# Kernel tuning notes

Hardware: AMD Instinct MI355X
Metric: run time of the kernel (lower is better)

The kernel has to match this reference:

```python
import jax, jax.numpy as jnp
import numpy as np

N = 100000
IN_F, C1, C2, C3, OUT_F = 64, 64, 64, 64, 8


def setup_inputs() -> dict:
    key = jax.random.key(0)
    ks = jax.random.split(key, 12)
    x = jax.random.normal(ks[0], (N, IN_F), dtype=jnp.float32)
    edge_index = jax.random.randint(ks[1], (2, 1600000), 0, N, dtype=jnp.int64)

    def lin(kw, kb, fi, fo):
        s = 1.0 / np.sqrt(fi)
        W = jax.random.uniform(kw, (fi, fo), jnp.float32, -s, s)
        b = jax.random.uniform(kb, (fo,), jnp.float32, -s, s)
        return W, b

    W1, b1 = lin(ks[2], ks[3], IN_F, C1)
    W2, b2 = lin(ks[4], ks[5], C1, C2)
    W3, b3 = lin(ks[6], ks[7], C2, C3)
    Wl, bl = lin(ks[8], ks[9], C3, OUT_F)
    return {"x": x, "edge_index": edge_index, "W1": W1, "b1": b1,
            "W2": W2, "b2": b2, "W3": W3, "b3": b3, "Wl": Wl, "bl": bl}


def _gcn_norm(edge_index, n):
    # add self loops, compute symmetric normalization D^-1/2 A D^-1/2
    loops = jnp.arange(n, dtype=edge_index.dtype)
    src = jnp.concatenate([edge_index[0], loops])
    dst = jnp.concatenate([edge_index[1], loops])
    deg = jax.ops.segment_sum(jnp.ones_like(dst, dtype=jnp.float32), dst, num_segments=n)
    dis = jnp.where(deg > 0, jax.lax.rsqrt(deg), 0.0)
    norm = dis[src] * dis[dst]  # [E+N]
    return src, dst, norm


def _gcn_layer(h, W, b, src, dst, norm, n):
    h = h @ W                                   # [N, Fout] small GEMM
    msg = h[src] * norm[:, None]                # gather + scale, [E+N, Fout]
    agg = jax.ops.segment_sum(msg, dst, num_segments=n)  # scatter-add
    return agg + b


def reference(x, edge_index, W1, b1, W2, b2, W3, b3, Wl, bl):
    n = x.shape[0]
    src, dst, norm = _gcn_norm(edge_index, n)
    h = jax.nn.relu(_gcn_layer(x, W1, b1, src, dst, norm, n))
    h = jax.nn.relu(_gcn_layer(h, W2, b2, src, dst, norm, n))
    h = jax.nn.relu(_gcn_layer(h, W3, b3, src, dst, norm, n))
    return h @ Wl + bl
```

## Files before the change

kernel.cpp:

```cpp
#include <hip/hip_runtime.h>
#include <hip/hip_fp16.h>

#define F 64
#define CHUNK 2048
#define BN 512
#define BSHIFT 9
#define CAP 20480

typedef int v4i __attribute__((ext_vector_type(4)));
typedef float fx4 __attribute__((ext_vector_type(4)));
typedef float v2f __attribute__((ext_vector_type(2)));
typedef _Float16 h8f __attribute__((ext_vector_type(8)));

union FB8 { uint4 u; h8f h; };
union FX4P { fx4 v; v2f p[2]; };

__global__ __launch_bounds__(256) void k_blkcnt(const int* __restrict__ dst,
                                                int* __restrict__ blkcnt,
                                                int E, int NB, int NBKT) {
    __shared__ int lcnt[256];
    int b = blockIdx.x, t = threadIdx.x;
    lcnt[t] = 0;
    __syncthreads();
    const v4i* d4 = (const v4i*)dst;
    int g0 = (b * CHUNK) >> 2;
    int E4 = E >> 2;
#pragma unroll
    for (int k = 0; k < 2; ++k) {
        int gi = g0 + k * 256 + t;
        if (gi < E4) {
            v4i q = __builtin_nontemporal_load(d4 + gi);
            atomicAdd(&lcnt[q.x >> BSHIFT], 1);
            atomicAdd(&lcnt[q.y >> BSHIFT], 1);
            atomicAdd(&lcnt[q.z >> BSHIFT], 1);
            atomicAdd(&lcnt[q.w >> BSHIFT], 1);
        }
    }
    __syncthreads();
    if (t < NBKT) blkcnt[t * NB + b] = lcnt[t];
}

__global__ __launch_bounds__(256) void k_bktscan(const int* __restrict__ blkcnt,
                                                 int* __restrict__ blkoff,
                                                 int* __restrict__ bkttot, int NB) {
    __shared__ int s[256];
    __shared__ int running;
    int seg = blockIdx.x;
    int t = threadIdx.x;
    if (t == 0) running = 0;
    __syncthreads();
    for (int base = 0; base < NB; base += 256) {
        int i = base + t;
        int v = (i < NB) ? blkcnt[seg * NB + i] : 0;
        s[t] = v;
        __syncthreads();
        for (int off = 1; off < 256; off <<= 1) {
            int x = (t >= off) ? s[t - off] : 0;
            __syncthreads();
            s[t] += x;
            __syncthreads();
        }
        int rbase = running;
        if (i < NB) blkoff[seg * NB + i] = rbase + s[t] - v;
        int ctot = s[255];
        __syncthreads();
        if (t == 0) running = rbase + ctot;
        __syncthreads();
    }
    if (t == 0) bkttot[seg] = running;
}

__global__ void k_sb(const int* __restrict__ bkttot, int* __restrict__ sb, int NBKT) {
    __shared__ int s[256];
    int t = threadIdx.x;
    int v = (t < NBKT) ? bkttot[t] : 0;
    s[t] = v;
    __syncthreads();
    for (int off = 1; off < 256; off <<= 1) {
        int x = (t >= off) ? s[t - off] : 0;
        __syncthreads();
        s[t] += x;
        __syncthreads();
    }
    if (t < NBKT) sb[t] = s[t] - v;
    if (t == NBKT - 1) sb[NBKT] = s[t];
}

__global__ __launch_bounds__(256) void k_stage2(const int* __restrict__ src,
                                                const int* __restrict__ dst,
                                                const int* __restrict__ blkoff,
                                                const int* __restrict__ sb,
                                                unsigned* __restrict__ stage,
                                                int E, int NB, int NBKT) {
    __shared__ int lcnt[256];
    __shared__ int lbase[257];
    __shared__ int obase[256];
    __shared__ int s[256];
    __shared__ unsigned rec[CHUNK];
    __shared__ unsigned char binof[CHUNK];
    int b = blockIdx.x, t = threadIdx.x;
    lcnt[t] = 0;
    __syncthreads();
    const v4i* d4 = (const v4i*)dst;
    const v4i* s4 = (const v4i*)src;
    int g0 = (b * CHUNK) >> 2;
    int E4 = E >> 2;
    int myseg[8], myrank[8];
    unsigned myrec[8];
#pragma unroll
    for (int k = 0; k < 2; ++k) {
        int gi = g0 + k * 256 + t;
        bool ok = gi < E4;
        v4i qd = {0, 0, 0, 0}, qs = {0, 0, 0, 0};
        if (ok) {
            qd = __builtin_nontemporal_load(d4 + gi);
            qs = __builtin_nontemporal_load(s4 + gi);
        }
        int dd[4] = {qd.x, qd.y, qd.z, qd.w};
        int ss[4] = {qs.x, qs.y, qs.z, qs.w};
#pragma unroll
        for (int j = 0; j < 4; ++j) {
            int idx = k * 4 + j;
            myseg[idx] = -1;
            if (ok) {
                int sg = dd[j] >> BSHIFT;
                myseg[idx] = sg;
                myrank[idx] = atomicAdd(&lcnt[sg], 1);
                myrec[idx] = ((unsigned)(dd[j] & (BN - 1)) << 17) | (unsigned)ss[j];
            }
        }
    }
    __syncthreads();
    int v = lcnt[t];
    s[t] = v;
    __syncthreads();
    for (int off = 1; off < 256; off <<= 1) {
        int x = (t >= off) ? s[t - off] : 0;
        __syncthreads();
        s[t] += x;
        __syncthreads();
    }
    lbase[t] = s[t] - v;
    if (t == 255) lbase[256] = s[255];
    obase[t] = (t < NBKT) ? sb[t] + blkoff[t * NB + b] : 0;
    __syncthreads();
#pragma unroll
    for (int k = 0; k < 8; ++k) {
        if (myseg[k] >= 0) {
            int p = lbase[myseg[k]] + myrank[k];
            rec[p] = myrec[k];
            binof[p] = (unsigned char)myseg[k];
        }
    }
    __syncthreads();
    int tot = lbase[256];
    for (int j = t; j < tot; j += 256) {
        int sg = binof[j];
        stage[obase[sg] + (j - lbase[sg])] = rec[j];
    }
}

__global__ __launch_bounds__(1024) void k_bincount(const unsigned* __restrict__ stage,
                                                   const int* __restrict__ sb,
                                                   int* __restrict__ count,
                                                   float* __restrict__ dis,
                                                   int* __restrict__ padtot, int n) {
    __shared__ int lc[BN];
    int bkt = blockIdx.x, t = threadIdx.x;
    int nb0 = bkt << BSHIFT;
    if (t < BN) lc[t] = 0;
    __syncthreads();
    int r0 = sb[bkt], r1 = sb[bkt + 1];
    for (int j = r0 + t; j < r1; j += 1024) {
        unsigned r = stage[j];
        atomicAdd(&lc[r >> 17], 1);
    }
    __syncthreads();
    int pv = 0;
    if (t < BN) {
        int node = nb0 + t;
        int cv = lc[t];
        if (node < n) {
            count[node] = cv;
            dis[node] = rsqrtf((float)(cv + 1));
            pv = (cv + 3) & ~3;
        }
    }
    __syncthreads();
    if (t < BN) lc[t] = pv;
    __syncthreads();
    for (int off = 256; off > 0; off >>= 1) {
        if (t < off) lc[t] += lc[t + off];
        __syncthreads();
    }
    if (t == 0) padtot[bkt] = lc[0];
}

__global__ void k_sb2(const int* __restrict__ padtot, int* __restrict__ rbase,
                      int* __restrict__ row_start, int NBKT, int n) {
    __shared__ int s[256];
    int t = threadIdx.x;
    int v = (t < NBKT) ? padtot[t] : 0;
    s[t] = v;
    __syncthreads();
    for (int off = 1; off < 256; off <<= 1) {
        int x = (t >= off) ? s[t - off] : 0;
        __syncthreads();
        s[t] += x;
        __syncthreads();
    }
    if (t < NBKT) rbase[t] = s[t] - v;
    if (t == NBKT - 1) { rbase[NBKT] = s[t]; row_start[n] = s[t]; }
}

__global__ __launch_bounds__(512) void k_binfill(const unsigned* __restrict__ stage,
                                                 const int* __restrict__ sb,
                                                 const int* __restrict__ count,
                                                 const int* __restrict__ rbase,
                                                 int* __restrict__ row_start,
                                                 int* __restrict__ csr, int n) {
    __shared__ int lcur[BN];
    __shared__ int sc[BN];
    __shared__ int buf[CAP];
    int bkt = blockIdx.x, t = threadIdx.x;
    int nb0 = bkt << BSHIFT;
    int node = nb0 + t;
    int pv = (node < n) ? ((count[node] + 3) & ~3) : 0;
    sc[t] = pv;
    __syncthreads();
    for (int off = 1; off < BN; off <<= 1) {
        int x = (t >= off) ? sc[t - off] : 0;
        __syncthreads();
        sc[t] += x;
        __syncthreads();
    }
    int excl = sc[t] - pv;
    int w0 = rbase[bkt];
    int wlen = sc[BN - 1];
    lcur[t] = excl;
    if (node < n) row_start[node] = w0 + excl;
    for (int j = t; j < wlen && j < CAP; j += 512) buf[j] = n;
    __syncthreads();
    int r0 = sb[bkt], r1 = sb[bkt + 1];
    for (int j = r0 + t; j < r1; j += 512) {
        unsigned r = stage[j];
        int p = atomicAdd(&lcur[r >> 17], 1);
        if (p < CAP) buf[p] = (int)(r & 0x1FFFFu);
    }
    __syncthreads();
    for (int j = t; j < wlen && j < CAP; j += 512) csr[w0 + j] = buf[j];
}

__global__ void k_prep(const float4* __restrict__ x4, const float* __restrict__ dis,
                       uint2* __restrict__ hs, uint2* __restrict__ hs2, int n) {
    int i = blockIdx.x * blockDim.x + threadIdx.x;
    int tot = (n + 1) * 16;
    if (i < tot) {
        int row = i >> 4;
        float dv = 0.0f;
        float4 v = make_float4(0.f, 0.f, 0.f, 0.f);
        if (row < n) { dv = dis[row]; v = x4[i]; }
        __half2 h01 = __floats2half2_rn(dv * v.x, dv * v.y);
        __half2 h23 = __floats2half2_rn(dv * v.z, dv * v.w);
        uint2 u;
        u.x = *(unsigned*)&h01;
        u.y = *(unsigned*)&h23;
        hs[i] = u;
    } else if (i < tot + 16) {
        hs2[(size_t)n * 16 + (i - tot)] = make_uint2(0u, 0u);
    }
}

__global__ __launch_bounds__(256) void k_layer(const __half* __restrict__ hin,
        const float* __restrict__ W, const float* __restrict__ b,
        const int* __restrict__ row_start, const int* __restrict__ csr,
        const float* __restrict__ dis, __half* __restrict__ hout,
        int n, int scale_out) {
    __shared__ char lds_all[16384];
    int tid = threadIdx.x;
    int lane = tid & 63;
    int wv = tid >> 6;
    int r0 = (blockIdx.x * 4 + wv) << 4;
    if (r0 >= n) return;
    char* myLds = lds_all + (wv << 12);
    const _Float16* hp = (const _Float16*)hin;

    int r_  = lane & 15;
    int g4  = lane >> 4;
    int l31 = lane & 31;

    int lo = row_start[r0 + r_];
    int hi = row_start[r0 + r_ + 1];
    int s0 = __shfl(lo, 0);
    int s4 = __shfl(hi, 15);
    int NBb = (s4 - s0 + 31) >> 5;
    unsigned deg = (unsigned)(hi - lo);

    fx4 acc0 = {0.f, 0.f, 0.f, 0.f};
    fx4 acc1 = acc0, acc2 = acc0, acc3 = acc0;

    auto ldnodes = [&](int i) -> int {
        if (i < NBb) {
            int slot = s0 + (i << 5) + l31;
            int nd = csr[slot];
            return (slot < s4) ? nd : n;
        }
        return (l31 < 16) ? (r0 + l31) : n;
    };

#define LOADFRAG(F0, F1, F2, F3, NDS) { \
    _Pragma("unroll") \
    for (int j = 0; j < 8; ++j) { \
        int ndj = __shfl((NDS), 8 * g4 + j); \
        const _Float16* rp = hp + (((size_t)(unsigned)ndj) << 6) + r_; \
        F0.h[j] = rp[0]; \
        F1.h[j] = rp[16]; \
        F2.h[j] = rp[32]; \
        F3.h[j] = rp[48]; \
    } \
}

#define SMFMA(TT, F0, F1, F2, F3) { \
    unsigned w[4]; \
    if ((TT) < NBb) { \
        unsigned u0 = (unsigned)(s0 + ((TT) << 5) + (g4 << 3)) - (unsigned)lo; \
        w[0] = ((u0     ) < deg ? 0x3C00u : 0u) | ((u0 + 1u) < deg ? 0x3C000000u : 0u); \
        w[1] = ((u0 + 2u) < deg ? 0x3C00u : 0u) | ((u0 + 3u) < deg ? 0x3C000000u : 0u); \
        w[2] = ((u0 + 4u) < deg ? 0x3C00u : 0u) | ((u0 + 5u) < deg ? 0x3C000000u : 0u); \
        w[3] = ((u0 + 6u) < deg ? 0x3C00u : 0u) | ((u0 + 7u) < deg ? 0x3C000000u : 0u); \
    } else { \
        int k0 = g4 << 3; \
        w[0] = ((k0    ) == r_ ? 0x3C00u : 0u) | ((k0 + 1) == r_ ? 0x3C000000u : 0u); \
        w[1] = ((k0 + 2) == r_ ? 0x3C00u : 0u) | ((k0 + 3) == r_ ? 0x3C000000u : 0u); \
        w[2] = ((k0 + 4) == r_ ? 0x3C00u : 0u) | ((k0 + 5) == r_ ? 0x3C000000u : 0u); \
        w[3] = ((k0 + 6) == r_ ? 0x3C00u : 0u) | ((k0 + 7) == r_ ? 0x3C000000u : 0u); \
    } \
    FB8 af; af.u = make_uint4(w[0], w[1], w[2], w[3]); \
    acc0 = __builtin_amdgcn_mfma_f32_16x16x32_f16(af.h, F0.h, acc0, 0, 0, 0); \
    acc1 = __builtin_amdgcn_mfma_f32_16x16x32_f16(af.h, F1.h, acc1, 0, 0, 0); \
    acc2 = __builtin_amdgcn_mfma_f32_16x16x32_f16(af.h, F2.h, acc2, 0, 0, 0); \
    acc3 = __builtin_amdgcn_mfma_f32_16x16x32_f16(af.h, F3.h, acc3, 0, 0, 0); \
}

    FB8 A0, A1, A2, A3, B0, B1, B2, B3;
    int ndA, ndB;
    {
        int nd0 = ldnodes(0);
        LOADFRAG(A0, A1, A2, A3, nd0)
        ndA = ldnodes(1);
        ndB = ldnodes(2);
    }

    for (int t = 0; ; t += 2) {
        LOADFRAG(B0, B1, B2, B3, ndA)
        ndA = ldnodes(t + 3);
        SMFMA(t, A0, A1, A2, A3)
        if (t + 1 > NBb) break;
        LOADFRAG(A0, A1, A2, A3, ndB)
        ndB = ldnodes(t + 4);
        SMFMA(t + 1, B0, B1, B2, B3)
        if (t + 2 > NBb) break;
    }
#undef LOADFRAG
#undef SMFMA

    float* T = (float*)myLds;
#define TSTORE(S, A) { \
    int fb_ = ((16 * (S) + r_) << 4) + (g4 << 2); \
    *(fx4*)(T + fb_) = A; }
    TSTORE(0, acc0) TSTORE(1, acc1) TSTORE(2, acc2) TSTORE(3, acc3)
#undef TSTORE

    float bb_ = b[lane];
    v2f yv2[8];
#pragma unroll
    for (int k = 0; k < 8; ++k) { yv2[k].x = 0.f; yv2[k].y = 0.f; }
    const float* Wp = W + lane;
#pragma unroll 4
    for (int f = 0; f < 64; ++f) {
        float w = Wp[f << 6];
        v2f wv; wv.x = w; wv.y = w;
        const float* Tf = T + (f << 4);
        FX4P d0, d1, d2, d3;
        d0.v = *(const fx4*)(Tf);
        d1.v = *(const fx4*)(Tf + 4);
        d2.v = *(const fx4*)(Tf + 8);
        d3.v = *(const fx4*)(Tf + 12);
        yv2[0] += d0.p[0] * wv;  yv2[1] += d0.p[1] * wv;
        yv2[2] += d1.p[0] * wv;  yv2[3] += d1.p[1] * wv;
        yv2[4] += d2.p[0] * wv;  yv2[5] += d2.p[1] * wv;
        yv2[6] += d3.p[0] * wv;  yv2[7] += d3.p[1] * wv;
    }

#pragma unroll
    for (int r = 0; r < 16; ++r) {
        float yvr = (r & 1) ? yv2[r >> 1].y : yv2[r >> 1].x;
        float dd = dis[r0 + r];
        float y = fmaxf(yvr * dd + bb_, 0.f);
        if (scale_out) y *= dd;
        hout[((size_t)(r0 + r) << 6) + lane] = __float2half(y);
    }
}

__global__ __launch_bounds__(256) void k_final(const __half* __restrict__ h,
                                               const float* __restrict__ Wl,
                                               const float* __restrict__ bl,
                                               float* __restrict__ out, int n) {
    __shared__ float Ws[F * 8];
    __shared__ float bs[8];
    int tid = threadIdx.x;
    Ws[tid] = Wl[tid];
    Ws[tid + 256] = Wl[tid + 256];
    if (tid < 8) bs[tid] = bl[tid];
    __syncthreads();
    int idx = blockIdx.x * 256 + tid;
    if (idx >= n * 8) return;
    int row = idx >> 3;
    int o = idx & 7;
    const __half* hr = h + (size_t)row * F;
    float acc = bs[o];
#pragma unroll
    for (int k = 0; k < F; ++k) acc = fmaf(__half2float(hr[k]), Ws[k * 8 + o], acc);
    out[idx] = acc;
}

extern "C" void kernel_launch(void* const* d_in, const int* in_sizes, int n_in,
                              void* d_out, int out_size, void* d_ws, size_t ws_size,
                              hipStream_t stream) {
    const float* x  = (const float*)d_in[0];
    const int*   ei = (const int*)d_in[1];
    const float* W1 = (const float*)d_in[2];
    const float* b1 = (const float*)d_in[3];
    const float* W2 = (const float*)d_in[4];
    const float* b2 = (const float*)d_in[5];
    const float* W3 = (const float*)d_in[6];
    const float* b3 = (const float*)d_in[7];
    const float* Wl = (const float*)d_in[8];
    const float* bl = (const float*)d_in[9];
    float* out = (float*)d_out;

    int n = in_sizes[0] / F;
    int E = in_sizes[1] / 2;
    const int* src = ei;
    const int* dst = ei + E;

    int np   = (n + 256) & ~255;
    int cap  = E + 3 * n + 64;
    int NB   = (E + CHUNK - 1) / CHUNK;
    int NBKT = (n + BN - 1) >> BSHIFT;

    int*      count     = (int*)d_ws;
    int*      row_start = count + np;
    int*      blkcnt    = row_start + np;
    int*      blkoff    = blkcnt + 256 * NB;
    int*      bkttot    = blkoff + 256 * NB;
    int*      sb        = bkttot + 256;
    int*      padtot    = sb + 272;
    int*      rbase     = padtot + 256;
    float*    dis       = (float*)(rbase + 272);
    unsigned* stage     = (unsigned*)(dis + np);
    int*      csr       = (int*)(stage + ((E + 3) & ~3));
    __half*   buf1      = (__half*)(csr + ((cap + 3) & ~3));
    __half*   buf2      = buf1 + (size_t)(n + 1) * F;

    k_blkcnt<<<NB, 256, 0, stream>>>(dst, blkcnt, E, NB, NBKT);

    k_bktscan<<<NBKT, 256, 0, stream>>>(blkcnt, blkoff, bkttot, NB);
    k_sb<<<1, 256, 0, stream>>>(bkttot, sb, NBKT);
    k_stage2<<<NB, 256, 0, stream>>>(src, dst, blkoff, sb, stage, E, NB, NBKT);

    k_bincount<<<NBKT, 1024, 0, stream>>>(stage, sb, count, dis, padtot, n);
    k_sb2<<<1, 256, 0, stream>>>(padtot, rbase, row_start, NBKT, n);

    k_binfill<<<NBKT, 512, 0, stream>>>(stage, sb, count, rbase, row_start, csr, n);

    k_prep<<<((n + 1) * 16 + 16 + 255) / 256, 256, 0, stream>>>(
        (const float4*)x, dis, (uint2*)buf1, (uint2*)buf2, n);

    int nb_l = (n + 63) / 64;
    k_layer<<<nb_l, 256, 0, stream>>>(buf1, W1, b1, row_start, csr, dis, buf2, n, 1);
    k_layer<<<nb_l, 256, 0, stream>>>(buf2, W2, b2, row_start, csr, dis, buf1, n, 1);
    k_layer<<<nb_l, 256, 0, stream>>>(buf1, W3, b3, row_start, csr, dis, buf2, n, 0);

    k_final<<<(n * 8 + 255) / 256, 256, 0, stream>>>(buf2, Wl, bl, out, n);
}
```

Before: 264.8 us.

## Fuse CSR build kernels, use fixed per-bucket CSR slots, deepen layer prefetch

Drops the two single-block scan kernels by redoing the bucket-total scan inside k_stage2 and the new fused k_bins kernel. k_bins combines degree counting, CSR fill and feature prescaling, with each bucket writing into a fixed MAXB-sized CSR region, so no global padded-offset scan is needed. k_layer now derives each row's end from count and uses a three-deep rather than two-deep gather prefetch. k_final computes all 8 outputs per row with vectorized loads. The fixed MAXB capacity silently drops edges if a bucket exceeds it, and the deeper prefetch uses more registers.

New measurement: 316.9 us. 1.2x slower.

```diff
diff --git a/kernel.cpp b/kernel.cpp
--- a/kernel.cpp
+++ b/kernel.cpp
@@ -5,7 +5,7 @@
 #define CHUNK 2048
 #define BN 512
 #define BSHIFT 9
-#define CAP 20480
+#define MAXB 11264
 
 typedef int v4i __attribute__((ext_vector_type(4)));
 typedef float fx4 __attribute__((ext_vector_type(4)));
@@ -70,26 +70,10 @@
     if (t == 0) bkttot[seg] = running;
 }
 
-__global__ void k_sb(const int* __restrict__ bkttot, int* __restrict__ sb, int NBKT) {
-    __shared__ int s[256];
-    int t = threadIdx.x;
-    int v = (t < NBKT) ? bkttot[t] : 0;
-    s[t] = v;
-    __syncthreads();
-    for (int off = 1; off < 256; off <<= 1) {
-        int x = (t >= off) ? s[t - off] : 0;
-        __syncthreads();
-        s[t] += x;
-        __syncthreads();
-    }
-    if (t < NBKT) sb[t] = s[t] - v;
-    if (t == NBKT - 1) sb[NBKT] = s[t];
-}
-
 __global__ __launch_bounds__(256) void k_stage2(const int* __restrict__ src,
                                                 const int* __restrict__ dst,
                                                 const int* __restrict__ blkoff,
-                                                const int* __restrict__ sb,
+                                                const int* __restrict__ bkttot,
                                                 unsigned* __restrict__ stage,
                                                 int E, int NB, int NBKT) {
     __shared__ int lcnt[256];
@@ -142,7 +126,17 @@
     }
     lbase[t] = s[t] - v;
     if (t == 255) lbase[256] = s[255];
-    obase[t] = (t < NBKT) ? sb[t] + blkoff[t * NB + b] : 0;
+    int bv = (t < NBKT) ? bkttot[t] : 0;
+    __syncthreads();
+    s[t] = bv;
+    __syncthreads();
+    for (int off = 1; off < 256; off <<= 1) {
+        int x = (t >= off) ? s[t - off] : 0;
+        __syncthreads();
+        s[t] += x;
+        __syncthreads();
+    }
+    obase[t] = (t < NBKT) ? (s[t] - bv) + blkoff[t * NB + b] : 0;
     __syncthreads();
 #pragma unroll
     for (int k = 0; k < 8; ++k) {
@@ -160,72 +154,45 @@
     }
 }
 
-__global__ __launch_bounds__(1024) void k_bincount(const unsigned* __restrict__ stage,
-                                                   const int* __restrict__ sb,
-                                                   int* __restrict__ count,
-                                                   float* __restrict__ dis,
-                                                   int* __restrict__ padtot, int n) {
+__global__ __launch_bounds__(512) void k_bins(const unsigned* __restrict__ stage,
+        const int* __restrict__ bkttot, const float4* __restrict__ x4,
+        int* __restrict__ count, int* __restrict__ row_start,
+        float* __restrict__ dis, int* __restrict__ csr,
+        uint2* __restrict__ hs, uint2* __restrict__ hs2, int n, int NBKT) {
+    __shared__ int s[256];
+    __shared__ int sbv[257];
     __shared__ int lc[BN];
+    __shared__ int sc[BN];
+    __shared__ float fdis[BN];
+    __shared__ int buf[MAXB];
     int bkt = blockIdx.x, t = threadIdx.x;
     int nb0 = bkt << BSHIFT;
-    if (t < BN) lc[t] = 0;
-    __syncthreads();
-    int r0 = sb[bkt], r1 = sb[bkt + 1];
-    for (int j = r0 + t; j < r1; j += 1024) {
-        unsigned r = stage[j];
-        atomicAdd(&lc[r >> 17], 1);
-    }
-    __syncthreads();
+    int bv = 0;
+    if (t < 256) { bv = (t < NBKT) ? bkttot[t] : 0; s[t] = bv; }
+    __syncthreads();
+    for (int off = 1; off < 256; off <<= 1) {
+        int x = (t < 256 && t >= off) ? s[t - off] : 0;
+        __syncthreads();
+        if (t < 256) s[t] += x;
+        __syncthreads();
+    }
+    if (t < 256) { sbv[t] = s[t] - bv; if (t == 255) sbv[256] = s[255]; }
+    lc[t] = 0;
+    __syncthreads();
+    int r0 = sbv[bkt], r1 = sbv[bkt + 1];
+    for (int j = r0 + t; j < r1; j += 512) atomicAdd(&lc[stage[j] >> 17], 1);
+    __syncthreads();
+    int node = nb0 + t;
+    int cv = lc[t];
     int pv = 0;
-    if (t < BN) {
-        int node = nb0 + t;
-        int cv = lc[t];
-        if (node < n) {
-            count[node] = cv;
-            dis[node] = rsqrtf((float)(cv + 1));
-            pv = (cv + 3) & ~3;
-        }
-    }
-    __syncthreads();
-    if (t < BN) lc[t] = pv;
-    __syncthreads();
-    for (int off = 256; off > 0; off >>= 1) {
-        if (t < off) lc[t] += lc[t + off];
-        __syncthreads();
-    }
-    if (t == 0) padtot[bkt] = lc[0];
-}
-
-__global__ void k_sb2(const int* __restrict__ padtot, int* __restrict__ rbase,
-                      int* __restrict__ row_start, int NBKT, int n) {
-    __shared__ int s[256];
-    int t = threadIdx.x;
-    int v = (t < NBKT) ? padtot[t] : 0;
-    s[t] = v;
-    __syncthreads();
-    for (int off = 1; off < 256; off <<= 1) {
-        int x = (t >= off) ? s[t - off] : 0;
-        __syncthreads();
-        s[t] += x;
-        __syncthreads();
-    }
-    if (t < NBKT) rbase[t] = s[t] - v;
-    if (t == NBKT - 1) { rbase[NBKT] = s[t]; row_start[n] = s[t]; }
-}
-
-__global__ __launch_bounds__(512) void k_binfill(const unsigned* __restrict__ stage,
-                                                 const int* __restrict__ sb,
-                                                 const int* __restrict__ count,
-                                                 const int* __restrict__ rbase,
-                                                 int* __restrict__ row_start,
-                                                 int* __restrict__ csr, int n) {
-    __shared__ int lcur[BN];
-    __shared__ int sc[BN];
-    __shared__ int buf[CAP];
-    int bkt = blockIdx.x, t = threadIdx.x;
-    int nb0 = bkt << BSHIFT;
-    int node = nb0 + t;
-    int pv = (node < n) ? ((count[node] + 3) & ~3) : 0;
+    float dval = 0.f;
+    if (node < n) {
+        count[node] = cv;
+        dval = rsqrtf((float)(cv + 1));
+        dis[node] = dval;
+        pv = (cv + 3) & ~3;
+    }
+    fdis[t] = dval;
     sc[t] = pv;
     __syncthreads();
     for (int off = 1; off < BN; off <<= 1) {
@@ -235,47 +202,41 @@
         __syncthreads();
     }
     int excl = sc[t] - pv;
-    int w0 = rbase[bkt];
     int wlen = sc[BN - 1];
-    lcur[t] = excl;
-    if (node < n) row_start[node] = w0 + excl;
-    for (int j = t; j < wlen && j < CAP; j += 512) buf[j] = n;
-    __syncthreads();
-    int r0 = sb[bkt], r1 = sb[bkt + 1];
+    if (node < n) row_start[node] = bkt * MAXB + excl;
+    lc[t] = excl;
+    for (int j = t; j < wlen && j < MAXB; j += 512) buf[j] = n;
+    __syncthreads();
     for (int j = r0 + t; j < r1; j += 512) {
         unsigned r = stage[j];
-        int p = atomicAdd(&lcur[r >> 17], 1);
-        if (p < CAP) buf[p] = (int)(r & 0x1FFFFu);
-    }
-    __syncthreads();
-    for (int j = t; j < wlen && j < CAP; j += 512) csr[w0 + j] = buf[j];
-}
-
-__global__ void k_prep(const float4* __restrict__ x4, const float* __restrict__ dis,
-                       uint2* __restrict__ hs, uint2* __restrict__ hs2, int n) {
-    int i = blockIdx.x * blockDim.x + threadIdx.x;
-    int tot = (n + 1) * 16;
-    if (i < tot) {
-        int row = i >> 4;
-        float dv = 0.0f;
+        int p = atomicAdd(&lc[r >> 17], 1);
+        if (p < MAXB) buf[p] = (int)(r & 0x1FFFFu);
+    }
+    __syncthreads();
+    int cbase = bkt * MAXB;
+    for (int j = t; j < wlen && j < MAXB; j += 512) csr[cbase + j] = buf[j];
+    for (int ii = t; ii < (BN << 4); ii += 512) {
+        int loc = ii >> 4;
+        int node2 = nb0 + loc;
+        int c = ii & 15;
+        float dv = 0.f;
         float4 v = make_float4(0.f, 0.f, 0.f, 0.f);
-        if (row < n) { dv = dis[row]; v = x4[i]; }
+        if (node2 < n) { dv = fdis[loc]; v = x4[(size_t)node2 * 16 + c]; }
         __half2 h01 = __floats2half2_rn(dv * v.x, dv * v.y);
         __half2 h23 = __floats2half2_rn(dv * v.z, dv * v.w);
         uint2 u;
         u.x = *(unsigned*)&h01;
         u.y = *(unsigned*)&h23;
-        hs[i] = u;
-    } else if (i < tot + 16) {
-        hs2[(size_t)n * 16 + (i - tot)] = make_uint2(0u, 0u);
+        if (node2 <= n) hs[(size_t)node2 * 16 + c] = u;
+        if (node2 == n) hs2[(size_t)n * 16 + c] = make_uint2(0u, 0u);
     }
 }
 
 __global__ __launch_bounds__(256) void k_layer(const __half* __restrict__ hin,
         const float* __restrict__ W, const float* __restrict__ b,
-        const int* __restrict__ row_start, const int* __restrict__ csr,
-        const float* __restrict__ dis, __half* __restrict__ hout,
-        int n, int scale_out) {
+        const int* __restrict__ row_start, const int* __restrict__ count,
+        const int* __restrict__ csr, const float* __restrict__ dis,
+        __half* __restrict__ hout, int n, int scale_out) {
     __shared__ char lds_all[16384];
     int tid = threadIdx.x;
     int lane = tid & 63;
@@ -290,7 +251,8 @@
     int l31 = lane & 31;
 
     int lo = row_start[r0 + r_];
-    int hi = row_start[r0 + r_ + 1];
+    int cnt_ = count[r0 + r_];
+    int hi = lo + ((cnt_ + 3) & ~3);
     int s0 = __shfl(lo, 0);
     int s4 = __shfl(hi, 15);
     int NBb = (s4 - s0 + 31) >> 5;
@@ -342,24 +304,29 @@
     acc3 = __builtin_amdgcn_mfma_f32_16x16x32_f16(af.h, F3.h, acc3, 0, 0, 0); \
 }
 
-    FB8 A0, A1, A2, A3, B0, B1, B2, B3;
-    int ndA, ndB;
+    FB8 A0, A1, A2, A3, B0, B1, B2, B3, C0, C1, C2, C3;
+    int ndX, ndY, ndZ;
     {
-        int nd0 = ldnodes(0);
-        LOADFRAG(A0, A1, A2, A3, nd0)
-        ndA = ldnodes(1);
-        ndB = ldnodes(2);
-    }
-
-    for (int t = 0; ; t += 2) {
-        LOADFRAG(B0, B1, B2, B3, ndA)
-        ndA = ldnodes(t + 3);
+        int nd = ldnodes(0);
+        LOADFRAG(A0, A1, A2, A3, nd)
+        nd = ldnodes(1);
+        LOADFRAG(B0, B1, B2, B3, nd)
+        ndX = ldnodes(2); ndY = ldnodes(3); ndZ = ldnodes(4);
+    }
+
+    for (int t = 0; ; t += 3) {
+        LOADFRAG(C0, C1, C2, C3, ndX)
+        ndX = ldnodes(t + 5);
         SMFMA(t, A0, A1, A2, A3)
         if (t + 1 > NBb) break;
-        LOADFRAG(A0, A1, A2, A3, ndB)
-        ndB = ldnodes(t + 4);
+        LOADFRAG(A0, A1, A2, A3, ndY)
+        ndY = ldnodes(t + 6);
         SMFMA(t + 1, B0, B1, B2, B3)
         if (t + 2 > NBb) break;
+        LOADFRAG(B0, B1, B2, B3, ndZ)
+        ndZ = ldnodes(t + 7);
+        SMFMA(t + 2, C0, C1, C2, C3)
+        if (t + 3 > NBb) break;
     }
 #undef LOADFRAG
 #undef SMFMA
@@ -413,15 +380,31 @@
     Ws[tid + 256] = Wl[tid + 256];
     if (tid < 8) bs[tid] = bl[tid];
     __syncthreads();
-    int idx = blockIdx.x * 256 + tid;
-    if (idx >= n * 8) return;
-    int row = idx >> 3;
-    int o = idx & 7;
-    const __half* hr = h + (size_t)row * F;
-    float acc = bs[o];
-#pragma unroll
-    for (int k = 0; k < F; ++k) acc = fmaf(__half2float(hr[k]), Ws[k * 8 + o], acc);
-    out[idx] = acc;
+    int row = blockIdx.x * 256 + tid;
+    if (row >= n) return;
+    const uint2* hr = (const uint2*)(h + (size_t)row * F);
+    float acc[8];
+#pragma unroll
+    for (int o = 0; o < 8; ++o) acc[o] = bs[o];
+#pragma unroll
+    for (int k4 = 0; k4 < 16; ++k4) {
+        uint2 u = hr[k4];
+        float2 f01 = __half22float2(*(__half2*)&u.x);
+        float2 f23 = __half22float2(*(__half2*)&u.y);
+        const float* w0 = Ws + (k4 * 4) * 8;
+#pragma unroll
+        for (int o = 0; o < 8; ++o) {
+            float a = acc[o];
+            a = fmaf(f01.x, w0[o], a);
+            a = fmaf(f01.y, w0[8 + o], a);
+            a = fmaf(f23.x, w0[16 + o], a);
+            a = fmaf(f23.y, w0[24 + o], a);
+            acc[o] = a;
+        }
+    }
+    float4* op = (float4*)(out + (size_t)row * 8);
+    op[0] = make_float4(acc[0], acc[1], acc[2], acc[3]);
+    op[1] = make_float4(acc[4], acc[5], acc[6], acc[7]);
 }
 
 extern "C" void kernel_launch(void* const* d_in, const int* in_sizes, int n_in,
@@ -445,7 +428,6 @@
     const int* dst = ei + E;
 
     int np   = (n + 256) & ~255;
-    int cap  = E + 3 * n + 64;
     int NB   = (E + CHUNK - 1) / CHUNK;
     int NBKT = (n + BN - 1) >> BSHIFT;
 
@@ -454,33 +436,25 @@
     int*      blkcnt    = row_start + np;
     int*      blkoff    = blkcnt + 256 * NB;
     int*      bkttot    = blkoff + 256 * NB;
-    int*      sb        = bkttot + 256;
-    int*      padtot    = sb + 272;
-    int*      rbase     = padtot + 256;
-    float*    dis       = (float*)(rbase + 272);
+    float*    dis       = (float*)(bkttot + 272);
     unsigned* stage     = (unsigned*)(dis + np);
     int*      csr       = (int*)(stage + ((E + 3) & ~3));
-    __half*   buf1      = (__half*)(csr + ((cap + 3) & ~3));
+    __half*   buf1      = (__half*)(csr + NBKT * MAXB + 64);
     __half*   buf2      = buf1 + (size_t)(n + 1) * F;
 
     k_blkcnt<<<NB, 256, 0, stream>>>(dst, blkcnt, E, NB, NBKT);
 
     k_bktscan<<<NBKT, 256, 0, stream>>>(blkcnt, blkoff, bkttot, NB);
-    k_sb<<<1, 256, 0, stream>>>(bkttot, sb, NBKT);
-    k_stage2<<<NB, 256, 0, stream>>>(src, dst, blkoff, sb, stage, E, NB, NBKT);
-
-    k_bincount<<<NBKT, 1024, 0, stream>>>(stage, sb, count, dis, padtot, n);
-    k_sb2<<<1, 256, 0, stream>>>(padtot, rbase, row_start, NBKT, n);
-
-    k_binfill<<<NBKT, 512, 0, stream>>>(stage, sb, count, rbase, row_start, csr, n);
-
-    k_prep<<<((n + 1) * 16 + 16 + 255) / 256, 256, 0, stream>>>(
-        (const float4*)x, dis, (uint2*)buf1, (uint2*)buf2, n);
+    k_stage2<<<NB, 256, 0, stream>>>(src, dst, blkoff, bkttot, stage, E, NB, NBKT);
+
+    k_bins<<<NBKT, 512, 0, stream>>>(stage, bkttot, (const float4*)x, count,
+                                     row_start, dis, csr, (uint2*)buf1,
+                                     (uint2*)buf2, n, NBKT);
 
     int nb_l = (n + 63) / 64;
-    k_layer<<<nb_l, 256, 0, stream>>>(buf1, W1, b1, row_start, csr, dis, buf2, n, 1);
-    k_layer<<<nb_l, 256, 0, stream>>>(buf2, W2, b2, row_start, csr, dis, buf1, n, 1);
-    k_layer<<<nb_l, 256, 0, stream>>>(buf1, W3, b3, row_start, csr, dis, buf2, n, 0);
-
-    k_final<<<(n * 8 + 255) / 256, 256, 0, stream>>>(buf2, Wl, bl, out, n);
-}
+    k_layer<<<nb_l, 256, 0, stream>>>(buf1, W1, b1, row_start, count, csr, dis, buf2, n, 1);
+    k_layer<<<nb_l, 256, 0, stream>>>(buf2, W2, b2, row_start, count, csr, dis, buf1, n, 1);
+    k_layer<<<nb_l, 256, 0, stream>>>(buf1, W3, b3, row_start, count, csr, dis, buf2, n, 0);
+
+    k_final<<<(n + 255) / 256, 256, 0, stream>>>(buf2, Wl, bl, out, n);
+}
```
